# Kernel tuning notes

Measured on AMD Instinct MI355X. Metric: run time of the kernel, lower is better.

## Reference

```python
import jax, jax.numpy as jnp
import numpy as np

NUM_OBJ = 3
MIN_OBJ_SCALE = 0.1
MAX_OBJ_SCALE = 0.8
MIN_Y_SCALE = 0.75
MAX_Y_SCALE = 1.25
OBJ_POS_BOUND = 0.9
EPS_FIX = 0.095
BIG = 1e12


def setup_inputs() -> dict:
    key = jax.random.key(0)
    k1, k2, k3 = jax.random.split(key, 3)
    n, T, C, H, W = 64, 32, 3, 64, 64
    x = jax.random.normal(k1, (n, T, C, H, W), dtype=jnp.float32)
    d = C * H * W
    W_enc = jax.random.normal(k2, (d, NUM_OBJ * 8), dtype=jnp.float32) / np.sqrt(d).astype(np.float32)
    b_enc = jax.random.normal(k3, (NUM_OBJ * 8,), dtype=jnp.float32) * 0.01
    return {"x": x, "W_enc": W_enc, "b_enc": b_enc}


def _constrain_zp_mean(zp):
    # zp: (nTo, 8) -> mean (nTo, 4). std branch is discarded by forward().
    zm = jnp.concatenate([jax.nn.sigmoid(zp[:, 0:2]), 2.0 * jax.nn.sigmoid(zp[:, 2:4]) - 1.0], -1)
    set_max = jnp.array([[MAX_OBJ_SCALE - MIN_OBJ_SCALE, MAX_Y_SCALE - MIN_Y_SCALE, OBJ_POS_BOUND, OBJ_POS_BOUND]], dtype=zp.dtype)
    set_min = jnp.array([[MIN_OBJ_SCALE, MIN_Y_SCALE, 0.0, 0.0]], dtype=zp.dtype)
    return zm * set_max + set_min


def _greedy_assign(errors):
    # errors: (n, o, o). Greedy row-by-row argmin, masking out used columns with BIG,
    # exactly as the torch fault-fix loop does via scatter of 1e12.
    n, o, _ = errors.shape
    def step(used, i):
        e = errors[:, i, :] + used * BIG
        j = jnp.argmin(e, -1)
        used = used + jax.nn.one_hot(j, o, dtype=errors.dtype)
        return used, j
    _, js = jax.lax.scan(step, jnp.zeros((n, o), errors.dtype), jnp.arange(o))
    return jnp.moveaxis(js, 0, 1)  # (n, o)


def _match_objects(z):
    # z: (n, T, o, 4). Sequential greedy matching over time.
    def step(prev, z_t):
        curr = jax.lax.stop_gradient(z_t[:, :, 2:4])          # (n, o, 2)
        prv = jax.lax.stop_gradient(prev[:, :, 2:4])          # (n, o, 2)
        errors = jnp.sum((prv[:, :, None, :] - curr[:, None, :, :]) ** 2, -1)  # (n, i, j)
        idx = jnp.argmin(errors, -1)                          # (n, o)
        # fault = assignment is not a permutation (num_obj==3 check from source)
        ok = jnp.all(idx[:, 1:] != idx[:, :-1], -1) & (idx[:, 0] != idx[:, 2])
        gidx = _greedy_assign(errors)
        idx = jnp.where(ok[:, None], idx, gidx)
        match = jnp.take_along_axis(z_t, idx[:, :, None], axis=1)
        return match, match
    z0 = z[:, 0]
    _, rest = jax.lax.scan(step, z0, jnp.moveaxis(z[:, 1:], 1, 0))
    return jnp.concatenate([z0[:, None], jnp.moveaxis(rest, 0, 1)], 1)


def _fix_supair(z):
    # z: (n, T, o, 4). Replace isolated position jumps with neighbor average.
    n, T, o, d = z.shape
    diffs = jax.lax.stop_gradient(jnp.abs(z[:, 1:, :, :2] - z[:, :-1, :, :2]))
    zpad2 = jnp.zeros((n, 1, o, 2), z.dtype)
    prev = jnp.concatenate([zpad2, diffs], 1)
    after = jnp.concatenate([diffs, zpad2], 1)
    mask = (prev > EPS_FIX) & (after > EPS_FIX)               # (n, T, o, 2)
    zpad = jnp.zeros((n, 1, o, d), z.dtype)
    smooth = jnp.concatenate([zpad, (z[:, :-2] + z[:, 2:]) / 2, zpad], 1)
    mask_full = jnp.concatenate((d // 2) * [mask], -1)        # (n, T, o, 4)
    return jnp.where(mask_full, smooth, z)


def reference(x, W_enc, b_enc):
    n, T = x.shape[0], x.shape[1]
    # encoder: per-frame linear to (num_obj, 8) z-parameters
    zp = x.reshape(n * T, -1) @ W_enc + b_enc                  # (nT, o*8)
    zm = _constrain_zp_mean(zp.reshape(-1, 8))                 # (nTo, 4)
    z = zm.reshape(n, T, NUM_OBJ, 4)
    z = _match_objects(z)
    z = _fix_supair(z)
    # v_from_state
    v = z[:, 1:, :, 2:] - z[:, :-1, :, 2:]
    zf = jnp.concatenate([z[:, 1:], v], -1)                    # (n, T-1, o, 6)
    zf = jnp.concatenate([jnp.zeros_like(zf[:, 0:1]), zf], 1)  # (n, T, o, 6)
    zf = zf[:, 1:, :, 2:]                                      # (n, T-1, o, 4)
    zf = jnp.concatenate([(zf[..., :2] + 1) / 2 * 10, zf[..., 2:] / 2 * 10], -1)
    zf = jnp.concatenate([zf[..., :2] / 5, zf[..., 2:] * 2], -1)
    return zf
```

## Files before the change

kernel.cpp:

```cpp
#include <hip/hip_runtime.h>

#define N_B   64
#define T_S   32
#define DIM   12288
#define ROWS  2048
#define NCOL  12
#define RPW   4
#define WAVES 4
#define RPB   (RPW * WAVES)
#define KSPL  16
#define KSEG  (DIM / KSPL)
#define JSTEP (KSEG / 256)

__global__ __launch_bounds__(256) void k_gemm(const float* __restrict__ x,
                                              const float* __restrict__ W,
                                              float* __restrict__ part) {
    __shared__ float wt[NCOL * KSEG];
    const int rb   = blockIdx.x >> 4;
    const int sg   = blockIdx.x & 15;
    const int tid  = threadIdx.x;
    const int wave = tid >> 6;
    const int lane = tid & 63;
    const int r0   = rb * RPB + wave * RPW;
    const int k00  = sg * KSEG;

#pragma unroll
    for (int it = 0; it < 9; ++it) {
        const int flat = tid + it * 256;
        const int k    = flat / 3;
        const int g    = flat - 3 * k;
        const float4 wv = *(const float4*)(W + (size_t)(k00 + k) * 24 + g * 8);
        float* d = wt + (g * 4) * KSEG + k;
        d[0 * KSEG] = wv.x;
        d[1 * KSEG] = wv.y;
        d[2 * KSEG] = wv.z;
        d[3 * KSEG] = wv.w;
    }

    float4 xv[JSTEP][RPW];
#pragma unroll
    for (int j = 0; j < JSTEP; ++j)
#pragma unroll
        for (int r = 0; r < RPW; ++r)
            xv[j][r] = *(const float4*)(x + (size_t)(r0 + r) * DIM + k00 + j * 256 + lane * 4);

    __syncthreads();

    float acc[RPW][NCOL];
#pragma unroll
    for (int r = 0; r < RPW; ++r)
#pragma unroll
        for (int c = 0; c < NCOL; ++c) acc[r][c] = 0.f;

#pragma unroll
    for (int j = 0; j < JSTEP; ++j) {
        const int kl = j * 256 + lane * 4;
#pragma unroll
        for (int c = 0; c < NCOL; ++c) {
            const float4 wv = *(const float4*)(wt + c * KSEG + kl);
#pragma unroll
            for (int r = 0; r < RPW; ++r)
                acc[r][c] += xv[j][r].x * wv.x + xv[j][r].y * wv.y +
                             xv[j][r].z * wv.z + xv[j][r].w * wv.w;
        }
    }

#pragma unroll
    for (int r = 0; r < RPW; ++r)
#pragma unroll
        for (int c = 0; c < NCOL; ++c) {
            float v = acc[r][c];
            v += __shfl_xor(v, 32, 64);
            v += __shfl_xor(v, 16, 64);
            v += __shfl_xor(v, 8, 64);
            v += __shfl_xor(v, 4, 64);
            v += __shfl_xor(v, 2, 64);
            v += __shfl_xor(v, 1, 64);
            acc[r][c] = v;
        }

    __syncthreads();
    float* red = wt;
    if (lane == 0) {
#pragma unroll
        for (int r = 0; r < RPW; ++r)
#pragma unroll
            for (int c = 0; c < NCOL; ++c)
                red[(wave * RPW + r) * NCOL + c] = acc[r][c];
    }
    __syncthreads();

    if (tid < RPB * NCOL)
        part[(size_t)sg * (ROWS * NCOL) + (size_t)rb * (RPB * NCOL) + tid] = red[tid];
}

__global__ __launch_bounds__(256) void k_reduce(const float* __restrict__ part,
                                                const float* __restrict__ b_enc,
                                                float* __restrict__ zbuf) {
    const int rc = blockIdx.x * 256 + threadIdx.x;
    float s = 0.f;
#pragma unroll
    for (int i = 0; i < KSPL; ++i) s += part[(size_t)i * (ROWS * NCOL) + rc];

    const int row = rc / NCOL;
    const int c   = rc - row * NCOL;
    const int o   = c >> 2;
    const int cp  = c & 3;
    s += b_enc[o * 8 + cp];
    const float sg = 1.f / (1.f + expf(-s));
    float v;
    if (cp == 0)      v = sg * 0.7f + 0.1f;
    else if (cp == 1) v = sg * 0.5f + 0.75f;
    else              v = (2.f * sg - 1.f) * 0.9f;
    zbuf[rc] = v;
}

__global__ __launch_bounds__(64) void k_post(const float* __restrict__ zbuf,
                                             float* __restrict__ out) {
    __shared__ float z[T_S * NCOL];
    __shared__ float zm[T_S * NCOL];
    __shared__ float zf[T_S * NCOL];
    __shared__ int   perm[T_S];
    const int b   = blockIdx.x;
    const int tid = threadIdx.x;

#pragma unroll
    for (int i = 0; i < 6; ++i)
        z[tid + 64 * i] = zbuf[b * 384 + tid + 64 * i];
    __syncthreads();

    if (tid == 0) {
        float px0 = z[2],  py0 = z[3];
        float px1 = z[6],  py1 = z[7];
        float px2 = z[10], py2 = z[11];
        for (int t = 1; t < T_S; ++t) {
            const int base = t * 12;
            const float cx0 = z[base + 2],  cy0 = z[base + 3];
            const float cx1 = z[base + 6],  cy1 = z[base + 7];
            const float cx2 = z[base + 10], cy2 = z[base + 11];

            float dx, dy;
            dx = px0 - cx0; dy = py0 - cy0; const float e00 = dx * dx + dy * dy;
            dx = px0 - cx1; dy = py0 - cy1; const float e01 = dx * dx + dy * dy;
            dx = px0 - cx2; dy = py0 - cy2; const float e02 = dx * dx + dy * dy;
            dx = px1 - cx0; dy = py1 - cy0; const float e10 = dx * dx + dy * dy;
            dx = px1 - cx1; dy = py1 - cy1; const float e11 = dx * dx + dy * dy;
            dx = px1 - cx2; dy = py1 - cy2; const float e12 = dx * dx + dy * dy;
            dx = px2 - cx0; dy = py2 - cy0; const float e20 = dx * dx + dy * dy;
            dx = px2 - cx1; dy = py2 - cy1; const float e21 = dx * dx + dy * dy;
            dx = px2 - cx2; dy = py2 - cy2; const float e22 = dx * dx + dy * dy;

            auto amin3 = [](float a0, float a1, float a2) {
                int j = 0; float e = a0;
                if (a1 < e) { e = a1; j = 1; }
                if (a2 < e) { j = 2; }
                return j;
            };
            int i0 = amin3(e00, e01, e02);
            int i1 = amin3(e10, e11, e12);
            int i2 = amin3(e20, e21, e22);
            const bool ok = (i1 != i0) && (i2 != i1) && (i0 != i2);
            if (!ok) {
                float u0 = 0.f, u1 = 0.f, u2 = 0.f;
                i0 = amin3(e00, e01, e02);
                if (i0 == 0) u0 = 1.f; else if (i0 == 1) u1 = 1.f; else u2 = 1.f;
                i1 = amin3(e10 + u0 * 1e12f, e11 + u1 * 1e12f, e12 + u2 * 1e12f);
                if (i1 == 0) u0 = 1.f; else if (i1 == 1) u1 = 1.f; else u2 = 1.f;
                i2 = amin3(e20 + u0 * 1e12f, e21 + u1 * 1e12f, e22 + u2 * 1e12f);
            }
            perm[t] = i0 * 9 + i1 * 3 + i2;
            px0 = (i0 == 0) ? cx0 : (i0 == 1) ? cx1 : cx2;
            py0 = (i0 == 0) ? cy0 : (i0 == 1) ? cy1 : cy2;
            px1 = (i1 == 0) ? cx0 : (i1 == 1) ? cx1 : cx2;
            py1 = (i1 == 0) ? cy0 : (i1 == 1) ? cy1 : cy2;
            px2 = (i2 == 0) ? cx0 : (i2 == 1) ? cx1 : cx2;
            py2 = (i2 == 0) ? cy0 : (i2 == 1) ? cy1 : cy2;
        }
    }
    __syncthreads();

#pragma unroll
    for (int ii = 0; ii < 6; ++ii) {
        const int i  = tid + 64 * ii;
        const int t  = i / 12;
        const int j  = i - t * 12;
        const int k  = j >> 2;
        const int ch = j & 3;
        int p = k;
        if (t > 0) {
            const int code = perm[t];
            p = (k == 0) ? code / 9 : (k == 1) ? (code % 9) / 3 : code % 3;
        }
        zm[i] = z[t * 12 + p * 4 + ch];
    }
    __syncthreads();

#pragma unroll
    for (int ii = 0; ii < 6; ++ii) {
        const int i  = tid + 64 * ii;
        const int t  = i / 12;
        const int j  = i - t * 12;
        const int o  = j >> 2;
        const int cc = j & 1;
        const int mb = o * 4 + cc;
        const float pd = (t >= 1)  ? fabsf(zm[t * 12 + mb] - zm[(t - 1) * 12 + mb]) : 0.f;
        const float ad = (t <= 30) ? fabsf(zm[(t + 1) * 12 + mb] - zm[t * 12 + mb]) : 0.f;
        const bool  m  = (pd > 0.095f) && (ad > 0.095f);
        const float sm = (t >= 1 && t <= 30)
                             ? (zm[(t - 1) * 12 + j] + zm[(t + 1) * 12 + j]) * 0.5f
                             : 0.f;
        zf[i] = m ? sm : zm[t * 12 + j];
    }
    __syncthreads();

    for (int i = tid; i < 31 * 12; i += 64) {
        const int t  = i / 12;
        const int j  = i - t * 12;
        const int o  = j >> 2;
        const int c2 = j & 3;
        const int pb = o * 4 + 2 + (c2 & 1);
        float v;
        if (c2 < 2) v = zf[(t + 1) * 12 + pb] + 1.f;
        else        v = (zf[(t + 1) * 12 + pb] - zf[t * 12 + pb]) * 10.f;
        out[b * 372 + i] = v;
    }
}

extern "C" void kernel_launch(void* const* d_in, const int* in_sizes, int n_in,
                              void* d_out, int out_size, void* d_ws, size_t ws_size,
                              hipStream_t stream) {
    (void)in_sizes; (void)n_in; (void)out_size; (void)ws_size;
    const float* x     = (const float*)d_in[0];
    const float* W_enc = (const float*)d_in[1];
    const float* b_enc = (const float*)d_in[2];
    float* out  = (float*)d_out;

    float* zbuf = (float*)d_ws;
    float* part = zbuf + ROWS * NCOL;

    k_gemm  <<<(ROWS / RPB) * KSPL, 256, 0, stream>>>(x, W_enc, part);
    k_reduce<<<(ROWS * NCOL) / 256, 256, 0, stream>>>(part, b_enc, zbuf);
    k_post  <<<N_B, 64, 0, stream>>>(zbuf, out);
}
```

Measured before the change: 171.7 us.

## Restructure skinny GEMM with repacked weights, LDS-staged x tiles, and fused reduction

A new kernel repacks W into a per-wave layout of 3 used columns, dropping the unused std columns. The GEMM now gives each block 64 rows staged through a swizzled LDS buffer. Each lane owns one row and 3 output columns, with wave-uniform weight loads and register prefetch of the next x chunk. The split-K partial reduction and sigmoid constraint move into the post kernel, removing one launch. This trades the per-lane cross-wave shuffle reductions for more split-K partials (32) and an extra repack launch on every call.

After: 203.3 us. 1.18x slower.

```diff
diff --git a/kernel.cpp b/kernel.cpp
--- a/kernel.cpp
+++ b/kernel.cpp
@@ -1,121 +1,98 @@
 #include <hip/hip_runtime.h>
 
-#define N_B   64
-#define T_S   32
-#define DIM   12288
-#define ROWS  2048
-#define NCOL  12
-#define RPW   4
-#define WAVES 4
-#define RPB   (RPW * WAVES)
-#define KSPL  16
-#define KSEG  (DIM / KSPL)
-#define JSTEP (KSEG / 256)
-
-__global__ __launch_bounds__(256) void k_gemm(const float* __restrict__ x,
-                                              const float* __restrict__ W,
-                                              float* __restrict__ part) {
-    __shared__ float wt[NCOL * KSEG];
-    const int rb   = blockIdx.x >> 4;
-    const int sg   = blockIdx.x & 15;
+#define N_B    64
+#define T_S    32
+#define DIM    12288
+#define ROWS   2048
+#define NCOL   12
+#define KSPL   32
+#define KSEG   (DIM / KSPL)
+#define BK     128
+#define NCHUNK (KSEG / BK)
+#define RPBK   64
+
+__global__ __launch_bounds__(256) void k_repack(const float* __restrict__ W,
+                                                float* __restrict__ Wp) {
+    const int idx = blockIdx.x * 256 + threadIdx.x;
+    const int w   = idx / (DIM * 3);
+    const int rem = idx - w * (DIM * 3);
+    const int k   = rem / 3;
+    const int cc  = rem - k * 3;
+    const int c   = w * 3 + cc;
+    const int col = (c >> 2) * 8 + (c & 3);
+    Wp[idx] = W[(size_t)k * 24 + col];
+}
+
+__global__ __launch_bounds__(256) void k_gemm2(const float* __restrict__ x,
+                                               const float* __restrict__ Wp,
+                                               float* __restrict__ part) {
+    __shared__ float4 xt[RPBK * (BK / 4)];
     const int tid  = threadIdx.x;
-    const int wave = tid >> 6;
     const int lane = tid & 63;
-    const int r0   = rb * RPB + wave * RPW;
+    const int rb   = blockIdx.x >> 5;
+    const int sg   = blockIdx.x & 31;
+    const int r0   = rb * RPBK;
     const int k00  = sg * KSEG;
-
-#pragma unroll
-    for (int it = 0; it < 9; ++it) {
-        const int flat = tid + it * 256;
-        const int k    = flat / 3;
-        const int g    = flat - 3 * k;
-        const float4 wv = *(const float4*)(W + (size_t)(k00 + k) * 24 + g * 8);
-        float* d = wt + (g * 4) * KSEG + k;
-        d[0 * KSEG] = wv.x;
-        d[1 * KSEG] = wv.y;
-        d[2 * KSEG] = wv.z;
-        d[3 * KSEG] = wv.w;
-    }
-
-    float4 xv[JSTEP][RPW];
-#pragma unroll
-    for (int j = 0; j < JSTEP; ++j)
-#pragma unroll
-        for (int r = 0; r < RPW; ++r)
-            xv[j][r] = *(const float4*)(x + (size_t)(r0 + r) * DIM + k00 + j * 256 + lane * 4);
-
-    __syncthreads();
-
-    float acc[RPW][NCOL];
-#pragma unroll
-    for (int r = 0; r < RPW; ++r)
-#pragma unroll
-        for (int c = 0; c < NCOL; ++c) acc[r][c] = 0.f;
-
-#pragma unroll
-    for (int j = 0; j < JSTEP; ++j) {
-        const int kl = j * 256 + lane * 4;
-#pragma unroll
-        for (int c = 0; c < NCOL; ++c) {
-            const float4 wv = *(const float4*)(wt + c * KSEG + kl);
-#pragma unroll
-            for (int r = 0; r < RPW; ++r)
-                acc[r][c] += xv[j][r].x * wv.x + xv[j][r].y * wv.y +
-                             xv[j][r].z * wv.z + xv[j][r].w * wv.w;
-        }
-    }
-
-#pragma unroll
-    for (int r = 0; r < RPW; ++r)
-#pragma unroll
-        for (int c = 0; c < NCOL; ++c) {
-            float v = acc[r][c];
-            v += __shfl_xor(v, 32, 64);
-            v += __shfl_xor(v, 16, 64);
-            v += __shfl_xor(v, 8, 64);
-            v += __shfl_xor(v, 4, 64);
-            v += __shfl_xor(v, 2, 64);
-            v += __shfl_xor(v, 1, 64);
-            acc[r][c] = v;
-        }
-
-    __syncthreads();
-    float* red = wt;
-    if (lane == 0) {
-#pragma unroll
-        for (int r = 0; r < RPW; ++r)
-#pragma unroll
-            for (int c = 0; c < NCOL; ++c)
-                red[(wave * RPW + r) * NCOL + c] = acc[r][c];
-    }
-    __syncthreads();
-
-    if (tid < RPB * NCOL)
-        part[(size_t)sg * (ROWS * NCOL) + (size_t)rb * (RPB * NCOL) + tid] = red[tid];
-}
-
-__global__ __launch_bounds__(256) void k_reduce(const float* __restrict__ part,
-                                                const float* __restrict__ b_enc,
-                                                float* __restrict__ zbuf) {
-    const int rc = blockIdx.x * 256 + threadIdx.x;
-    float s = 0.f;
-#pragma unroll
-    for (int i = 0; i < KSPL; ++i) s += part[(size_t)i * (ROWS * NCOL) + rc];
-
-    const int row = rc / NCOL;
-    const int c   = rc - row * NCOL;
-    const int o   = c >> 2;
-    const int cp  = c & 3;
-    s += b_enc[o * 8 + cp];
-    const float sg = 1.f / (1.f + expf(-s));
-    float v;
-    if (cp == 0)      v = sg * 0.7f + 0.1f;
-    else if (cp == 1) v = sg * 0.5f + 0.75f;
-    else              v = (2.f * sg - 1.f) * 0.9f;
-    zbuf[rc] = v;
-}
-
-__global__ __launch_bounds__(64) void k_post(const float* __restrict__ zbuf,
+    const int wv   = __builtin_amdgcn_readfirstlane(tid >> 6);
+
+    const float* wbase = Wp + (size_t)wv * (DIM * 3) + (size_t)k00 * 3;
+    const float* xb    = x + (size_t)r0 * DIM + k00;
+
+    float4 st[8];
+#pragma unroll
+    for (int i = 0; i < 8; ++i) {
+        const int f = tid + 256 * i;
+        st[i] = *(const float4*)(xb + (size_t)(f >> 5) * DIM + (f & 31) * 4);
+    }
+
+    float acc0 = 0.f, acc1 = 0.f, acc2 = 0.f;
+
+    for (int ch = 0; ch < NCHUNK; ++ch) {
+        __syncthreads();
+#pragma unroll
+        for (int i = 0; i < 8; ++i) {
+            const int f   = tid + 256 * i;
+            const int row = f >> 5;
+            const int c4  = (f & 31) ^ (row & 7);
+            xt[row * 32 + c4] = st[i];
+        }
+        __syncthreads();
+        if (ch + 1 < NCHUNK) {
+#pragma unroll
+            for (int i = 0; i < 8; ++i) {
+                const int f = tid + 256 * i;
+                st[i] = *(const float4*)(xb + (size_t)(f >> 5) * DIM +
+                                         (ch + 1) * BK + (f & 31) * 4);
+            }
+        }
+        const float* wc = wbase + ch * (BK * 3);
+#pragma unroll
+        for (int g = 0; g < 8; ++g) {
+            const float* wg = wc + g * 48;
+            float ws[48];
+#pragma unroll
+            for (int q = 0; q < 48; ++q) ws[q] = wg[q];
+#pragma unroll
+            for (int jj = 0; jj < 4; ++jj) {
+                const int j = g * 4 + jj;
+                const float4 xv = xt[lane * 32 + (j ^ (lane & 7))];
+                acc0 += xv.x * ws[jj*12 + 0] + xv.y * ws[jj*12 + 3] +
+                        xv.z * ws[jj*12 + 6] + xv.w * ws[jj*12 + 9];
+                acc1 += xv.x * ws[jj*12 + 1] + xv.y * ws[jj*12 + 4] +
+                        xv.z * ws[jj*12 + 7] + xv.w * ws[jj*12 + 10];
+                acc2 += xv.x * ws[jj*12 + 2] + xv.y * ws[jj*12 + 5] +
+                        xv.z * ws[jj*12 + 8] + xv.w * ws[jj*12 + 11];
+            }
+        }
+    }
+
+    float* p = part + (size_t)sg * (ROWS * NCOL) +
+               (size_t)(r0 + lane) * NCOL + wv * 3;
+    p[0] = acc0; p[1] = acc1; p[2] = acc2;
+}
+
+__global__ __launch_bounds__(64) void k_post(const float* __restrict__ part,
+                                             const float* __restrict__ b_enc,
                                              float* __restrict__ out) {
     __shared__ float z[T_S * NCOL];
     __shared__ float zm[T_S * NCOL];
@@ -125,8 +102,23 @@
     const int tid = threadIdx.x;
 
 #pragma unroll
-    for (int i = 0; i < 6; ++i)
-        z[tid + 64 * i] = zbuf[b * 384 + tid + 64 * i];
+    for (int ii = 0; ii < 6; ++ii) {
+        const int i = tid + 64 * ii;
+        float s = 0.f;
+#pragma unroll
+        for (int sgi = 0; sgi < KSPL; ++sgi)
+            s += part[(size_t)sgi * (ROWS * NCOL) + b * 384 + i];
+        const int c  = i % 12;
+        const int o  = c >> 2;
+        const int cp = c & 3;
+        s += b_enc[o * 8 + cp];
+        const float sgm = 1.f / (1.f + expf(-s));
+        float v;
+        if (cp == 0)      v = sgm * 0.7f + 0.1f;
+        else if (cp == 1) v = sgm * 0.5f + 0.75f;
+        else              v = (2.f * sgm - 1.f) * 0.9f;
+        z[i] = v;
+    }
     __syncthreads();
 
     if (tid == 0) {
@@ -235,10 +227,10 @@
     const float* b_enc = (const float*)d_in[2];
     float* out  = (float*)d_out;
 
-    float* zbuf = (float*)d_ws;
-    float* part = zbuf + ROWS * NCOL;
-
-    k_gemm  <<<(ROWS / RPB) * KSPL, 256, 0, stream>>>(x, W_enc, part);
-    k_reduce<<<(ROWS * NCOL) / 256, 256, 0, stream>>>(part, b_enc, zbuf);
-    k_post  <<<N_B, 64, 0, stream>>>(zbuf, out);
-}
+    float* part = (float*)d_ws;
+    float* Wp   = part + (size_t)KSPL * ROWS * NCOL;
+
+    k_repack<<<(4 * DIM * 3) / 256, 256, 0, stream>>>(W_enc, Wp);
+    k_gemm2 <<<(ROWS / RPBK) * KSPL, 256, 0, stream>>>(x, Wp, part);
+    k_post  <<<N_B, 64, 0, stream>>>(part, b_enc, out);
+}
```
